# Kernel tuning notes

Hardware: AMD Instinct MI355X
Metric: run time of the kernel (lower is better)

Reference implementation:

```python
import jax, jax.numpy as jnp
import numpy as np
import math

B, N, E = 1024, 128, 1024
IN_DIM, H, EDGE_DIM, L, OUT_DIM = 16, 128, 4, 4, 1


def setup_inputs() -> dict:
    key = jax.random.key(0)
    ks = jax.random.split(key, 32)
    def g(k, shape, scale):
        return jax.random.normal(k, shape, dtype=jnp.float32) * scale
    D_in = IN_DIM + 3
    s_in = 1.0 / math.sqrt(D_in)
    s_h = 1.0 / math.sqrt(H)
    inp = {
        'atom_types': jax.random.normal(ks[0], (B, N, IN_DIM), dtype=jnp.float32),
        'coords_spherical': jax.random.uniform(ks[1], (B, N, 3), dtype=jnp.float32),
        'edge_index': jax.random.randint(ks[2], (B, 2, E), 0, N, dtype=jnp.int32),
        'edge_attr': jax.random.uniform(ks[3], (B, E, EDGE_DIM), dtype=jnp.float32),
        # ComplexEmbedding: magnitude / phase linear maps
        'emb_Wm': g(ks[4], (D_in, H), s_in), 'emb_bm': jnp.zeros((H,), jnp.float32),
        'emb_Wp': g(ks[5], (D_in, H), s_in), 'emb_bp': jnp.zeros((H,), jnp.float32),
        # per-layer attention params (stacked over L layers)
        'Wq': g(ks[6], (L, H, H), s_h), 'bq': jnp.zeros((L, H), jnp.float32),
        'Wk': g(ks[7], (L, H, H), s_h), 'bk': jnp.zeros((L, H), jnp.float32),
        'Wvm': g(ks[8], (L, H, H), s_h), 'bvm': jnp.zeros((L, H), jnp.float32),
        'Wvp': g(ks[9], (L, H, H), s_h), 'bvp': jnp.zeros((L, H), jnp.float32),
        # EdgeBiasProjection: edge_attr -> scalar bias, plus learned distance penalty
        'We': g(ks[10], (L, EDGE_DIM, 1), 0.5), 'be': jnp.zeros((L, 1), jnp.float32),
        'dist_scale': jnp.full((L,), -0.5, jnp.float32),
        # LayerNorm over magnitude
        'ln_g': jnp.ones((L, H), jnp.float32), 'ln_b': jnp.zeros((L, H), jnp.float32),
        # RealProjection: concat(real, imag) -> hidden
        'rp_W': g(ks[11], (2 * H, H), 1.0 / math.sqrt(2 * H)), 'rp_b': jnp.zeros((H,), jnp.float32),
        # out_head: Linear(2H, H) -> SiLU -> Linear(H, out_dim)
        'h1_W': g(ks[12], (2 * H, H), 1.0 / math.sqrt(2 * H)), 'h1_b': jnp.zeros((H,), jnp.float32),
        'h2_W': g(ks[13], (H, OUT_DIM), s_h), 'h2_b': jnp.zeros((OUT_DIM,), jnp.float32),
    }
    return inp


def reference(atom_types, coords_spherical, edge_index, edge_attr,
              emb_Wm, emb_bm, emb_Wp, emb_bp,
              Wq, bq, Wk, bk, Wvm, bvm, Wvp, bvp,
              We, be, dist_scale, ln_g, ln_b,
              rp_W, rp_b, h1_W, h1_b, h2_W, h2_b):
    n_layers = Wq.shape[0]
    hidden = Wq.shape[-1]
    scale = 1.0 / math.sqrt(hidden)  # CAMBIO 1: sqrt(D) scaling

    def mol_fwd(feats, sph, ei, ea):
        n = feats.shape[0]
        x = jnp.concatenate([feats, sph], axis=-1)          # [N, in_dim+3]
        mag = x @ emb_Wm + emb_bm                            # [N, H]
        ph = x @ emb_Wp + emb_bp                             # [N, H]
        for l in range(n_layers):
            q = mag @ Wq[l] + bq[l]
            k = mag @ Wk[l] + bk[l]
            vm = mag @ Wvm[l] + bvm[l]
            vp = ph @ Wvp[l] + bvp[l]
            scores = (q @ k.T) * scale                       # [N, N]
            # CAMBIO 3/7: edge_attr -> scalar bias + learned distance penalty
            bvals = (ea @ We[l] + be[l])[:, 0] + dist_scale[l] * ea[:, 0]  # [E]
            bias = jnp.zeros((n, n), scores.dtype).at[ei[0], ei[1]].add(bvals)
            attn = jax.nn.softmax(scores + bias, axis=-1)
            new_mag = attn @ vm + mag                        # residual
            new_ph = attn @ vp + ph                          # residual
            # CAMBIO 6: LayerNorm over magnitude only
            mu = new_mag.mean(-1, keepdims=True)
            var = ((new_mag - mu) ** 2).mean(-1, keepdims=True)
            mag = ln_g[l] * (new_mag - mu) * jax.lax.rsqrt(var + 1e-5) + ln_b[l]
            ph = new_ph
        # CAMBIO 4: RealProjection concat(real, imag)
        real = mag * jnp.cos(ph)
        imag = mag * jnp.sin(ph)
        atom_repr = jnp.concatenate([real, imag], axis=-1) @ rp_W + rp_b  # [N, H]
        # CAMBIO 2: mean + sum pooling
        return jnp.concatenate([atom_repr.mean(0), atom_repr.sum(0)], axis=-1)  # [2H]

    pooled = jax.vmap(mol_fwd)(atom_types, coords_spherical, edge_index, edge_attr)  # [B, 2H]
    h = jax.nn.silu(pooled @ h1_W + h1_b)
    return h @ h2_W + h2_b                                   # [B, out_dim]
```

## Files before the change

kernel.cpp:

```cpp
#include <hip/hip_runtime.h>
#include <math.h>


typedef __attribute__((ext_vector_type(8)))  short s16x8;
typedef __attribute__((ext_vector_type(16))) float f32x16;

#define STR  136
#define LOFS 17408
#define MFMA(a, b, c) __builtin_amdgcn_mfma_f32_32x32x16_bf16(a, b, c, 0, 0, 0)
#define ROWP(reg) (((reg) & 3) + (((reg) >> 2) << 3) + (h5 << 2))

__device__ __forceinline__ unsigned short bfhi(float x) {
  unsigned u = __float_as_uint(x);
  return (unsigned short)((u + 0x7FFFu + ((u >> 16) & 1u)) >> 16);
}
__device__ __forceinline__ float bf2f(unsigned short h) {
  return __uint_as_float(((unsigned)h) << 16);
}

__device__ __forceinline__ void stageB64(short* SH, const f32x16& acc, int row,
                                         int colbase, int h5, float scl) {
  #pragma unroll
  for (int q = 0; q < 4; ++q) {
    int col = colbase + 8 * q + 4 * h5;
    float v0 = acc[4*q+0] * scl, v1 = acc[4*q+1] * scl;
    float v2 = acc[4*q+2] * scl, v3 = acc[4*q+3] * scl;
    unsigned u01, u23;
    asm("v_cvt_pk_bf16_f32 %0, %1, %2" : "=v"(u01) : "v"(v0), "v"(v1));
    asm("v_cvt_pk_bf16_f32 %0, %1, %2" : "=v"(u23) : "v"(v2), "v"(v3));
    float r0 = v0 - __uint_as_float(u01 << 16);
    float r1 = v1 - __uint_as_float(u01 & 0xFFFF0000u);
    float r2 = v2 - __uint_as_float(u23 << 16);
    float r3 = v3 - __uint_as_float(u23 & 0xFFFF0000u);
    unsigned l01, l23;
    asm("v_cvt_pk_bf16_f32 %0, %1, %2" : "=v"(l01) : "v"(r0), "v"(r1));
    asm("v_cvt_pk_bf16_f32 %0, %1, %2" : "=v"(l23) : "v"(r2), "v"(r3));
    uint2 hi2; hi2.x = u01; hi2.y = u23;
    uint2 lo2; lo2.x = l01; lo2.y = l23;
    *(uint2*)(SH + row * STR + col) = hi2;
    *(uint2*)(SH + LOFS + row * STR + col) = lo2;
  }
}

__device__ __forceinline__ void gemmTW2(f32x16* acc, const short* W, const short* BH,
                                        int mtile, int kbN, int ttb, int l31, int h5,
                                        int lane) {
  const short* wp0 = W + (((mtile * 8) * 64 + lane) * 8);
  s16x8 ah = *(const s16x8*)wp0;
  s16x8 al = *(const s16x8*)(wp0 + 32768);
  #pragma unroll 1
  for (int kb = 0; kb < kbN; ++kb) {
    int nk = (kb + 1 < kbN) ? kb + 1 : kb;
    const short* np = W + (((mtile * 8 + nk) * 64 + lane) * 8);
    s16x8 nah = *(const s16x8*)np;
    s16x8 nal = *(const s16x8*)(np + 32768);
    int k0 = kb * 16 + 8 * h5;
    #pragma unroll
    for (int j = 0; j < 2; ++j) {
      int brow = 32 * (ttb + j) + l31;
      s16x8 bh = *(const s16x8*)(BH + brow * STR + k0);
      s16x8 bl = *(const s16x8*)(BH + LOFS + brow * STR + k0);
      acc[j] = MFMA(ah, bh, acc[j]);
      acc[j] = MFMA(ah, bl, acc[j]);
      acc[j] = MFMA(al, bh, acc[j]);
    }
    ah = nah; al = nal;
  }
}

__device__ __forceinline__ void gemmNW2(f32x16* acc, const short* AH, const short* W,
                                        int mblk, int ttb, int l31, int h5, int lane) {
  int arow = mblk + l31;
  const short* ap0 = AH + arow * STR + 8 * h5;
  s16x8 ah = *(const s16x8*)ap0;
  s16x8 al = *(const s16x8*)(ap0 + LOFS);
  #pragma unroll 1
  for (int kb = 0; kb < 8; ++kb) {
    int nk0 = ((kb < 7) ? kb + 1 : 7) * 16 + 8 * h5;
    s16x8 nah = *(const s16x8*)(AH + arow * STR + nk0);
    s16x8 nal = *(const s16x8*)(AH + LOFS + arow * STR + nk0);
    #pragma unroll
    for (int j = 0; j < 2; ++j) {
      const short* wp = W + ((((ttb + j) * 8 + kb) * 64 + lane) * 8);
      s16x8 bh = *(const s16x8*)wp;
      s16x8 bl = *(const s16x8*)(wp + 32768);
      acc[j] = MFMA(ah, bh, acc[j]);
      acc[j] = MFMA(ah, bl, acc[j]);
      acc[j] = MFMA(al, bh, acc[j]);
    }
    ah = nah; al = nal;
  }
}

__device__ __forceinline__ void gemmLL2(f32x16* acc, const short* AH, const short* BH,
                                        int mblk, int ttb, int l31, int h5) {
  int arow = mblk + l31;
  const short* ap0 = AH + arow * STR + 8 * h5;
  s16x8 ah = *(const s16x8*)ap0;
  s16x8 al = *(const s16x8*)(ap0 + LOFS);
  #pragma unroll 1
  for (int kb = 0; kb < 8; ++kb) {
    int nk0 = ((kb < 7) ? kb + 1 : 7) * 16 + 8 * h5;
    s16x8 nah = *(const s16x8*)(AH + arow * STR + nk0);
    s16x8 nal = *(const s16x8*)(AH + LOFS + arow * STR + nk0);
    int k0 = kb * 16 + 8 * h5;
    #pragma unroll
    for (int j = 0; j < 2; ++j) {
      int brow = 32 * (ttb + j) + l31;
      s16x8 bh = *(const s16x8*)(BH + brow * STR + k0);
      s16x8 bl = *(const s16x8*)(BH + LOFS + brow * STR + k0);
      acc[j] = MFMA(ah, bh, acc[j]);
      acc[j] = MFMA(ah, bl, acc[j]);
      acc[j] = MFMA(al, bh, acc[j]);
    }
    ah = nah; al = nal;
  }
}

__global__ __launch_bounds__(256)
void prep0_kernel(const float* __restrict__ Wq, const float* __restrict__ Wk,
                  const float* __restrict__ bq,
                  float* __restrict__ wprime, float* __restrict__ u) {
  __shared__ float WkS[128 * 129];
  __shared__ float WqS[32 * 129];
  int l = blockIdx.x >> 2, ablk = blockIdx.x & 3;
  int t = threadIdx.x;
  const float* wk = Wk + (size_t)l * 16384;
  const float* wq = Wq + (size_t)l * 16384 + ablk * 32 * 128;
  for (int idx = t; idx < 16384; idx += 256)
    WkS[(idx >> 7) * 129 + (idx & 127)] = wk[idx];
  for (int idx = t; idx < 4096; idx += 256)
    WqS[(idx >> 7) * 129 + (idx & 127)] = wq[idx];
  __syncthreads();
  int a = t >> 3, bs = t & 7;
  float acc[16];
  #pragma unroll
  for (int j = 0; j < 16; ++j) acc[j] = 0.f;
  for (int c = 0; c < 128; ++c) {
    float qa = WqS[a * 129 + c];
    #pragma unroll
    for (int j = 0; j < 16; ++j) acc[j] += qa * WkS[(8 * j + bs) * 129 + c];
  }
  float* dst = wprime + ((size_t)l * 128 + ablk * 32 + a) * 128;
  #pragma unroll
  for (int j = 0; j < 16; ++j) dst[8 * j + bs] = acc[j];
  if (ablk == 0 && t < 128) {
    float s = 0.f;
    const float* bql = bq + l * 128;
    for (int c = 0; c < 128; ++c) s += WkS[t * 129 + c] * bql[c];
    u[l * 128 + t] = 0.08838834764831845f * s;
  }
}

__global__ __launch_bounds__(512)
void prep_kernel(const float* __restrict__ wprime,
                 const float* __restrict__ Wvm, const float* __restrict__ Wvp,
                 const float* __restrict__ rp_W,
                 const float* __restrict__ emb_Wm, const float* __restrict__ emb_Wp,
                 short* __restrict__ ws) {
  int mid = blockIdx.x >> 2, hblk = blockIdx.x & 3;
  int kb = threadIdx.x >> 6, lane = threadIdx.x & 63;
  const float* src;
  int krows = 128;
  if (mid < 4)        src = wprime + (size_t)mid * 16384;
  else if (mid < 8)   src = Wvm + (size_t)(mid - 4) * 16384;
  else if (mid < 12)  src = Wvp + (size_t)(mid - 8) * 16384;
  else if (mid == 12) src = rp_W;
  else if (mid == 13) src = rp_W + 16384;
  else if (mid == 14) { src = emb_Wm; krows = 19; }
  else                { src = emb_Wp; krows = 19; }
  int h = hblk * 32 + (lane & 31);
  int kbase = kb * 16 + ((lane >> 5) << 3);
  s16x8 H, L;
  #pragma unroll
  for (int j = 0; j < 8; ++j) {
    int k = kbase + j;
    float v = (k < krows) ? src[(size_t)k * 128 + h] : 0.f;
    unsigned short hi = bfhi(v);
    H[j] = (short)hi;
    L[j] = (short)bfhi(v - bf2f(hi));
  }
  short* dst = ws + (size_t)mid * 65536 + ((hblk * 8 + kb) * 64 + lane) * 8;
  *(s16x8*)dst = H;
  *(s16x8*)(dst + 32768) = L;
}

__global__ __launch_bounds__(512, 2)
void cpt_kernel(const float* __restrict__ atom_types,
                const float* __restrict__ coords,
                const int*   __restrict__ edge_index,
                const float* __restrict__ edge_attr,
                const float* __restrict__ emb_bm, const float* __restrict__ emb_bp,
                const float* __restrict__ bvm, const float* __restrict__ bvp,
                const float* __restrict__ We,  const float* __restrict__ be,
                const float* __restrict__ dist_scale,
                const float* __restrict__ ln_g, const float* __restrict__ ln_b,
                const float* __restrict__ rp_b,
                const float* __restrict__ h1_W, const float* __restrict__ h1_b,
                const float* __restrict__ h2_W, const float* __restrict__ h2_b,
                const short* __restrict__ wpre, const float* __restrict__ uArr,
                float* __restrict__ out)
{
  __shared__ __align__(16) short R1s[34816];
  __shared__ __align__(16) short R2s[34816];
  __shared__ float SCa[512];
  __shared__ float SCb[512];

  const int t = threadIdx.x, b = blockIdx.x;
  const int w = t >> 6, lane = t & 63, l31 = lane & 31, h5 = lane >> 5;
  const int wm = w >> 1, ttb = (w & 1) << 1;
  const int mblk = wm << 5;
  const float scale = 0.08838834764831845f;

  if (t < 128) {
    const float* xr = atom_types + ((size_t)b * 128 + t) * 16;
    const float* cr = coords + ((size_t)b * 128 + t) * 3;
    float xv[19];
    float4 a0 = *(const float4*)xr,       a1 = *(const float4*)(xr + 4);
    float4 a2 = *(const float4*)(xr + 8), a3 = *(const float4*)(xr + 12);
    xv[0]=a0.x; xv[1]=a0.y; xv[2]=a0.z; xv[3]=a0.w;
    xv[4]=a1.x; xv[5]=a1.y; xv[6]=a1.z; xv[7]=a1.w;
    xv[8]=a2.x; xv[9]=a2.y; xv[10]=a2.z; xv[11]=a2.w;
    xv[12]=a3.x; xv[13]=a3.y; xv[14]=a3.z; xv[15]=a3.w;
    xv[16]=cr[0]; xv[17]=cr[1]; xv[18]=cr[2];
    #pragma unroll
    for (int k = 0; k < 32; ++k) {
      float v = (k < 19) ? xv[k] : 0.f;
      unsigned short hh = bfhi(v);
      R1s[t * STR + k] = (short)hh;
      R1s[LOFS + t * STR + k] = (short)bfhi(v - bf2f(hh));
    }
  }
  __syncthreads();

  f32x16 magT[2], phT[2];
  {
    #pragma unroll
    for (int reg = 0; reg < 16; ++reg) {
      float bm = emb_bm[32 * wm + ROWP(reg)];
      float bp = emb_bp[32 * wm + ROWP(reg)];
      #pragma unroll
      for (int j = 0; j < 2; ++j) { magT[j][reg] = bm; phT[j][reg] = bp; }
    }
    gemmTW2(magT, wpre + (size_t)14 * 65536, R1s, wm, 2, ttb, l31, h5, lane);
    gemmTW2(phT,  wpre + (size_t)15 * 65536, R1s, wm, 2, ttb, l31, h5, lane);
  }

  for (int l = 0; l < 4; ++l) {
    const short* wpP  = wpre + (size_t)l * 65536;
    const short* wvmP = wpre + (size_t)(4 + l) * 65536;
    const short* wvpP = wpre + (size_t)(8 + l) * 65536;
    float* Bf = (float*)R2s;

    __syncthreads();
    #pragma unroll
    for (int j = 0; j < 2; ++j)
      stageB64(R1s, magT[j], 32 * (ttb + j) + l31, mblk, h5, 1.f);
    {
      float4 z4 = make_float4(0.f, 0.f, 0.f, 0.f);
      #pragma unroll
      for (int k = 0; k < 8; ++k) *(float4*)(Bf + (t + 512 * k) * 4) = z4;
    }
    {
      float ur[16];
      #pragma unroll
      for (int reg = 0; reg < 16; ++reg) ur[reg] = uArr[l * 128 + 32 * wm + ROWP(reg)];
      #pragma unroll
      for (int j = 0; j < 2; ++j) {
        float p = 0.f;
        #pragma unroll
        for (int reg = 0; reg < 16; ++reg) p += magT[j][reg] * ur[reg];
        p += __shfl_xor(p, 32);
        if (h5 == 0) SCa[wm * 128 + 32 * (ttb + j) + l31] = p;
      }
    }
    __syncthreads();

    {
      float w0 = We[l*4], w1 = We[l*4+1], w2 = We[l*4+2], w3 = We[l*4+3];
      float bel = be[l], dsl = dist_scale[l];
      #pragma unroll
      for (int k = 0; k < 2; ++k) {
        int e = t + 512 * k;
        int e0 = edge_index[(size_t)b * 2048 + e];
        int e1 = edge_index[(size_t)b * 2048 + 1024 + e];
        float4 ea = *(const float4*)(edge_attr + ((size_t)b * 1024 + e) * 4);
        float bv = ea.x*w0 + ea.y*w1 + ea.z*w2 + ea.w*w3 + bel + dsl*ea.x;
        atomicAdd(&Bf[e1 * 128 + e0], bv);
      }
    }

    f32x16 accT[2];
    #pragma unroll
    for (int j = 0; j < 2; ++j)
      #pragma unroll
      for (int reg = 0; reg < 16; ++reg) accT[j][reg] = 0.f;
    gemmTW2(accT, wpP, R1s, wm, 8, ttb, l31, h5, lane);
    __syncthreads();

    f32x16 accS[2];
    {
      float vj[16];
      #pragma unroll
      for (int reg = 0; reg < 16; ++reg) {
        int jj = 32 * wm + ROWP(reg);
        vj[reg] = SCa[jj] + SCa[128 + jj] + SCa[256 + jj] + SCa[384 + jj];
      }
      #pragma unroll
      for (int j = 0; j < 2; ++j) {
        #pragma unroll
        for (int reg = 0; reg < 16; ++reg)
          accS[j][reg] = Bf[(32 * wm + ROWP(reg)) * 128 + 32 * (ttb + j) + l31] + vj[reg];
      }
    }
    __syncthreads();
    #pragma unroll
    for (int j = 0; j < 2; ++j)
      stageB64(R2s, accT[j], 32 * (ttb + j) + l31, mblk, h5, scale);
    __syncthreads();

    gemmLL2(accS, R1s, R2s, mblk, ttb, l31, h5);

    #pragma unroll
    for (int j = 0; j < 2; ++j) {
      float m = accS[j][0];
      #pragma unroll
      for (int reg = 1; reg < 16; ++reg) m = fmaxf(m, accS[j][reg]);
      m = fmaxf(m, __shfl_xor(m, 32));
      if (h5 == 0) SCa[wm * 128 + 32 * (ttb + j) + l31] = m;
    }
    __syncthreads();
    #pragma unroll
    for (int j = 0; j < 2; ++j) {
      int i = 32 * (ttb + j) + l31;
      float mg = fmaxf(fmaxf(SCa[i], SCa[128 + i]), fmaxf(SCa[256 + i], SCa[384 + i]));
      float s = 0.f;
      #pragma unroll
      for (int reg = 0; reg < 16; ++reg) {
        float e = __expf(accS[j][reg] - mg);
        accS[j][reg] = e; s += e;
      }
      s += __shfl_xor(s, 32);
      if (h5 == 0) SCb[wm * 128 + i] = s;
    }
    __syncthreads();
    #pragma unroll
    for (int j = 0; j < 2; ++j) {
      int i = 32 * (ttb + j) + l31;
      float sg = SCb[i] + SCb[128 + i] + SCb[256 + i] + SCb[384 + i];
      float inv = 1.f / sg;
      #pragma unroll
      for (int reg = 0; reg < 16; ++reg) accS[j][reg] *= inv;
    }
    #pragma unroll
    for (int j = 0; j < 2; ++j)
      stageB64(R2s, accS[j], 32 * (ttb + j) + l31, mblk, h5, 1.f);

    {
      f32x16 accVM[2];
      #pragma unroll
      for (int j = 0; j < 2; ++j) {
        float bv = bvm[l * 128 + 32 * (ttb + j) + l31];
        #pragma unroll
        for (int reg = 0; reg < 16; ++reg) accVM[j][reg] = bv;
      }
      gemmNW2(accVM, R1s, wvmP, mblk, ttb, l31, h5, lane);
      __syncthreads();
      #pragma unroll
      for (int j = 0; j < 2; ++j)
        stageB64(R1s, accVM[j], 32 * (ttb + j) + l31, mblk, h5, 1.f);
      __syncthreads();
    }

    f32x16 accM[2];
    #pragma unroll
    for (int j = 0; j < 2; ++j) accM[j] = magT[j];
    gemmLL2(accM, R1s, R2s, mblk, ttb, l31, h5);

    {
      #pragma unroll
      for (int j = 0; j < 2; ++j) {
        float s = 0.f, q = 0.f;
        #pragma unroll
        for (int reg = 0; reg < 16; ++reg) { float v = accM[j][reg]; s += v; q += v*v; }
        s += __shfl_xor(s, 32); q += __shfl_xor(q, 32);
        if (h5 == 0) {
          SCa[wm * 128 + 32 * (ttb + j) + l31] = s;
          SCb[wm * 128 + 32 * (ttb + j) + l31] = q;
        }
      }
      __syncthreads();
      #pragma unroll
      for (int reg = 0; reg < 16; ++reg) {
        float gv = ln_g[l * 128 + 32 * wm + ROWP(reg)];
        float bv = ln_b[l * 128 + 32 * wm + ROWP(reg)];
        #pragma unroll
        for (int j = 0; j < 2; ++j) {
          int i = 32 * (ttb + j) + l31;
          float s = SCa[i] + SCa[128 + i] + SCa[256 + i] + SCa[384 + i];
          float q = SCb[i] + SCb[128 + i] + SCb[256 + i] + SCb[384 + i];
          float mu = s * (1.f / 128.f);
          float var = q * (1.f / 128.f) - mu * mu;
          float inv = 1.f / sqrtf(var + 1e-5f);
          magT[j][reg] = gv * ((accM[j][reg] - mu) * inv) + bv;
        }
      }
    }
    #pragma unroll
    for (int j = 0; j < 2; ++j)
      stageB64(R1s, phT[j], 32 * (ttb + j) + l31, mblk, h5, 1.f);
    __syncthreads();

    {
      f32x16 accV[2];
      #pragma unroll
      for (int j = 0; j < 2; ++j) {
        float bv = bvp[l * 128 + 32 * (ttb + j) + l31];
        #pragma unroll
        for (int reg = 0; reg < 16; ++reg) accV[j][reg] = bv;
      }
      gemmNW2(accV, R1s, wvpP, mblk, ttb, l31, h5, lane);
      __syncthreads();
      #pragma unroll
      for (int j = 0; j < 2; ++j)
        stageB64(R1s, accV[j], 32 * (ttb + j) + l31, mblk, h5, 1.f);
      __syncthreads();
    }

    f32x16 accP[2];
    #pragma unroll
    for (int j = 0; j < 2; ++j) accP[j] = phT[j];
    gemmLL2(accP, R1s, R2s, mblk, ttb, l31, h5);
    #pragma unroll
    for (int j = 0; j < 2; ++j) phT[j] = accP[j];
  }

  f32x16 reT[2], imT[2];
  #pragma unroll
  for (int j = 0; j < 2; ++j)
    #pragma unroll
    for (int reg = 0; reg < 16; ++reg) {
      float s_, c_;
      __sincosf(phT[j][reg], &s_, &c_);
      reT[j][reg] = magT[j][reg] * c_;
      imT[j][reg] = magT[j][reg] * s_;
    }
  __syncthreads();
  #pragma unroll
  for (int j = 0; j < 2; ++j) {
    stageB64(R1s, reT[j], 32 * (ttb + j) + l31, mblk, h5, 1.f);
    stageB64(R2s, imT[j], 32 * (ttb + j) + l31, mblk, h5, 1.f);
  }
  __syncthreads();
  f32x16 accR[2];
  #pragma unroll
  for (int reg = 0; reg < 16; ++reg) {
    float bv = rp_b[32 * wm + ROWP(reg)];
    #pragma unroll
    for (int j = 0; j < 2; ++j) accR[j][reg] = bv;
  }
  gemmTW2(accR, wpre + (size_t)12 * 65536, R1s, wm, 8, ttb, l31, h5, lane);
  gemmTW2(accR, wpre + (size_t)13 * 65536, R2s, wm, 8, ttb, l31, h5, lane);

  {
    float cs[16];
    #pragma unroll
    for (int reg = 0; reg < 16; ++reg) {
      float s = accR[0][reg] + accR[1][reg];
      s += __shfl_xor(s, 16); s += __shfl_xor(s, 8);
      s += __shfl_xor(s, 4);  s += __shfl_xor(s, 2); s += __shfl_xor(s, 1);
      cs[reg] = s;
    }
    if (l31 == 0) {
      #pragma unroll
      for (int reg = 0; reg < 16; ++reg)
        SCa[(w & 1) * 128 + 32 * wm + ROWP(reg)] = cs[reg];
    }
  }
  __syncthreads();
  if (t < 128) {
    float acc = h1_b[t];
    for (int i = 0; i < 128; ++i) {
      float c = SCa[i] + SCa[128 + i];
      acc += c * (h1_W[(size_t)i * 128 + t] * (1.f / 128.f) +
                  h1_W[(size_t)(128 + i) * 128 + t]);
    }
    float hv = acc / (1.f + __expf(-acc));
    SCb[t] = hv * h2_W[t];
  }
  __syncthreads();
  if (t < 64) {
    float s2 = SCb[t] + SCb[64 + t];
    #pragma unroll
    for (int off = 32; off >= 1; off >>= 1) s2 += __shfl_xor(s2, off);
    if (t == 0) out[b] = s2 + h2_b[0];
  }
}

extern "C" void kernel_launch(void* const* d_in, const int* in_sizes, int n_in,
                              void* d_out, int out_size, void* d_ws, size_t ws_size,
                              hipStream_t stream) {
  const float* atom_types = (const float*)d_in[0];
  const float* coords     = (const float*)d_in[1];
  const int*   edge_index = (const int*)  d_in[2];
  const float* edge_attr  = (const float*)d_in[3];
  const float* emb_Wm = (const float*)d_in[4];
  const float* emb_bm = (const float*)d_in[5];
  const float* emb_Wp = (const float*)d_in[6];
  const float* emb_bp = (const float*)d_in[7];
  const float* Wq  = (const float*)d_in[8];
  const float* bq  = (const float*)d_in[9];
  const float* Wk  = (const float*)d_in[10];
  const float* bk  = (const float*)d_in[11];
  const float* Wvm = (const float*)d_in[12];
  const float* bvm = (const float*)d_in[13];
  const float* Wvp = (const float*)d_in[14];
  const float* bvp = (const float*)d_in[15];
  const float* We  = (const float*)d_in[16];
  const float* be  = (const float*)d_in[17];
  const float* dist_scale = (const float*)d_in[18];
  const float* ln_g = (const float*)d_in[19];
  const float* ln_b = (const float*)d_in[20];
  const float* rp_W = (const float*)d_in[21];
  const float* rp_b = (const float*)d_in[22];
  const float* h1_W = (const float*)d_in[23];
  const float* h1_b = (const float*)d_in[24];
  const float* h2_W = (const float*)d_in[25];
  const float* h2_b = (const float*)d_in[26];
  float* out = (float*)d_out;
  (void)bk;
  short* wpre   = (short*)d_ws;
  float* uArr   = (float*)((char*)d_ws + (size_t)16 * 131072);
  float* wprime = (float*)((char*)d_ws + (size_t)16 * 131072 + 2048);

  hipLaunchKernelGGL(prep0_kernel, dim3(16), dim3(256), 0, stream,
                     Wq, Wk, bq, wprime, uArr);
  hipLaunchKernelGGL(prep_kernel, dim3(64), dim3(512), 0, stream,
                     wprime, Wvm, Wvp, rp_W, emb_Wm, emb_Wp, wpre);
  hipLaunchKernelGGL(cpt_kernel, dim3(1024), dim3(512), 0, stream,
                     atom_types, coords, edge_index, edge_attr,
                     emb_bm, emb_bp,
                     bvm, bvp,
                     We, be, dist_scale, ln_g, ln_b,
                     rp_b, h1_W, h1_b, h2_W, h2_b,
                     (const short*)wpre, (const float*)uArr, out);
}
```

Baseline: 572.3 us.

## Overlap edge loads with barrier, online-softmax merge, split output head matvec

Edge index and attribute loads are now issued before the barrier and only the atomic adds follow it, so global latency can overlap the sync. The softmax computes per-wave local max and sum in one pass and merges the partials with exp rescaling, which removes one barrier and one LDS round trip per layer. The final head matvec is split across all 512 threads in four row segments with a reduction step, instead of running on 128 threads only. This adds extra exp calls and an extra barrier in the epilogue.

```diff
diff --git a/kernel.cpp b/kernel.cpp
--- a/kernel.cpp
+++ b/kernel.cpp
@@ -274,21 +274,24 @@
         if (h5 == 0) SCa[wm * 128 + 32 * (ttb + j) + l31] = p;
       }
     }
-    __syncthreads();
-
+    int e0h[2], e1h[2]; float bvh[2];
     {
       float w0 = We[l*4], w1 = We[l*4+1], w2 = We[l*4+2], w3 = We[l*4+3];
       float bel = be[l], dsl = dist_scale[l];
       #pragma unroll
       for (int k = 0; k < 2; ++k) {
         int e = t + 512 * k;
-        int e0 = edge_index[(size_t)b * 2048 + e];
-        int e1 = edge_index[(size_t)b * 2048 + 1024 + e];
+        e0h[k] = edge_index[(size_t)b * 2048 + e];
+        e1h[k] = edge_index[(size_t)b * 2048 + 1024 + e];
         float4 ea = *(const float4*)(edge_attr + ((size_t)b * 1024 + e) * 4);
-        float bv = ea.x*w0 + ea.y*w1 + ea.z*w2 + ea.w*w3 + bel + dsl*ea.x;
-        atomicAdd(&Bf[e1 * 128 + e0], bv);
-      }
-    }
+        bvh[k] = ea.x*w0 + ea.y*w1 + ea.z*w2 + ea.w*w3 + bel + dsl*ea.x;
+      }
+    }
+    __syncthreads();
+
+    #pragma unroll
+    for (int k = 0; k < 2; ++k)
+      atomicAdd(&Bf[e1h[k] * 128 + e0h[k]], bvh[k]);
 
     f32x16 accT[2];
     #pragma unroll
@@ -321,36 +324,37 @@
 
     gemmLL2(accS, R1s, R2s, mblk, ttb, l31, h5);
 
+    float mloc[2];
     #pragma unroll
     for (int j = 0; j < 2; ++j) {
       float m = accS[j][0];
       #pragma unroll
       for (int reg = 1; reg < 16; ++reg) m = fmaxf(m, accS[j][reg]);
       m = fmaxf(m, __shfl_xor(m, 32));
-      if (h5 == 0) SCa[wm * 128 + 32 * (ttb + j) + l31] = m;
+      mloc[j] = m;
+      float s = 0.f;
+      #pragma unroll
+      for (int reg = 0; reg < 16; ++reg) {
+        float e = __expf(accS[j][reg] - m);
+        accS[j][reg] = e; s += e;
+      }
+      s += __shfl_xor(s, 32);
+      if (h5 == 0) {
+        SCa[wm * 128 + 32 * (ttb + j) + l31] = m;
+        SCb[wm * 128 + 32 * (ttb + j) + l31] = s;
+      }
     }
     __syncthreads();
     #pragma unroll
     for (int j = 0; j < 2; ++j) {
       int i = 32 * (ttb + j) + l31;
-      float mg = fmaxf(fmaxf(SCa[i], SCa[128 + i]), fmaxf(SCa[256 + i], SCa[384 + i]));
-      float s = 0.f;
-      #pragma unroll
-      for (int reg = 0; reg < 16; ++reg) {
-        float e = __expf(accS[j][reg] - mg);
-        accS[j][reg] = e; s += e;
-      }
-      s += __shfl_xor(s, 32);
-      if (h5 == 0) SCb[wm * 128 + i] = s;
-    }
-    __syncthreads();
-    #pragma unroll
-    for (int j = 0; j < 2; ++j) {
-      int i = 32 * (ttb + j) + l31;
-      float sg = SCb[i] + SCb[128 + i] + SCb[256 + i] + SCb[384 + i];
-      float inv = 1.f / sg;
-      #pragma unroll
-      for (int reg = 0; reg < 16; ++reg) accS[j][reg] *= inv;
+      float m0 = SCa[i], m1 = SCa[128 + i], m2 = SCa[256 + i], m3 = SCa[384 + i];
+      float M = fmaxf(fmaxf(m0, m1), fmaxf(m2, m3));
+      float S = SCb[i]        * __expf(m0 - M) + SCb[128 + i] * __expf(m1 - M)
+              + SCb[256 + i]  * __expf(m2 - M) + SCb[384 + i] * __expf(m3 - M);
+      float f = __expf(mloc[j] - M) / S;
+      #pragma unroll
+      for (int reg = 0; reg < 16; ++reg) accS[j][reg] *= f;
     }
     #pragma unroll
     for (int j = 0; j < 2; ++j)
@@ -478,19 +482,26 @@
     }
   }
   __syncthreads();
+  {
+    int col = t & 127, seg = t >> 7;
+    float acc = (seg == 0) ? h1_b[col] : 0.f;
+    int i0 = seg * 32;
+    for (int i = i0; i < i0 + 32; ++i) {
+      float c = SCa[i] + SCa[128 + i];
+      acc += c * (h1_W[(size_t)i * 128 + col] * (1.f / 128.f) +
+                  h1_W[(size_t)(128 + i) * 128 + col]);
+    }
+    SCb[t] = acc;
+  }
+  __syncthreads();
   if (t < 128) {
-    float acc = h1_b[t];
-    for (int i = 0; i < 128; ++i) {
-      float c = SCa[i] + SCa[128 + i];
-      acc += c * (h1_W[(size_t)i * 128 + t] * (1.f / 128.f) +
-                  h1_W[(size_t)(128 + i) * 128 + t]);
-    }
-    float hv = acc / (1.f + __expf(-acc));
-    SCb[t] = hv * h2_W[t];
+    float a = SCb[t] + SCb[128 + t] + SCb[256 + t] + SCb[384 + t];
+    float hv = a / (1.f + __expf(-a));
+    SCa[t] = hv * h2_W[t];
   }
   __syncthreads();
   if (t < 64) {
-    float s2 = SCb[t] + SCb[64 + t];
+    float s2 = SCa[t] + SCa[64 + t];
     #pragma unroll
     for (int off = 32; off >= 1; off >>= 1) s2 += __shfl_xor(s2, off);
     if (t == 0) out[b] = s2 + h2_b[0];
```

New measurement: 561.1 us. About the same (-2.0%).
